# Kernel optimization log

Measured on AMD Instinct MI355X. Metric: run time of the kernel, lower is better.

Reference implementation:

```python
import jax, jax.numpy as jnp
import numpy as np

D_MODEL = 1024
N_HEADS = 16
D_HEAD = D_MODEL // N_HEADS
D_FF = 4096
BATCH = 2
SEQ = 2048
LN_EPS = 1e-5


def setup_inputs() -> dict:
    key = jax.random.key(0)
    ks = jax.random.split(key, 12)
    s = 1.0 / np.sqrt(D_MODEL)
    x = jax.random.normal(ks[0], (BATCH, SEQ, D_MODEL), dtype=jnp.float32)
    mask = jnp.broadcast_to(jnp.tril(jnp.ones((SEQ, SEQ), jnp.int32)), (BATCH, SEQ, SEQ))
    return {
        "x": x,
        "mask": mask,
        # per-head projections stacked: [H, D, Dh] (bias=False in source)
        "Wq": jax.random.normal(ks[1], (N_HEADS, D_MODEL, D_HEAD), jnp.float32) * s,
        "Wk": jax.random.normal(ks[2], (N_HEADS, D_MODEL, D_HEAD), jnp.float32) * s,
        "Wv": jax.random.normal(ks[3], (N_HEADS, D_MODEL, D_HEAD), jnp.float32) * s,
        "Wo": jax.random.normal(ks[4], (D_MODEL, D_MODEL), jnp.float32) * s,
        "ln1_w": jnp.ones((D_MODEL,), jnp.float32),
        "ln1_b": jnp.zeros((D_MODEL,), jnp.float32),
        "ln2_w": jnp.ones((D_MODEL,), jnp.float32),
        "ln2_b": jnp.zeros((D_MODEL,), jnp.float32),
        "W1": jax.random.normal(ks[5], (D_MODEL, D_FF), jnp.float32) * s,
        "b1": jnp.zeros((D_FF,), jnp.float32),
        "W2": jax.random.normal(ks[6], (D_FF, D_MODEL), jnp.float32) * (1.0 / np.sqrt(D_FF)),
        "b2": jnp.zeros((D_MODEL,), jnp.float32),
    }


def layer_norm(x, w, b):
    mu = jnp.mean(x, axis=-1, keepdims=True)
    var = jnp.var(x, axis=-1, keepdims=True)
    return (x - mu) * jax.lax.rsqrt(var + LN_EPS) * w + b


def reference(x, mask, Wq, Wk, Wv, Wo, ln1_w, ln1_b, ln2_w, ln2_b, W1, b1, W2, b2):
    # pre-LN masked self-attention
    h = layer_norm(x, ln1_w, ln1_b)
    q = jnp.einsum("bsd,hde->bhse", h, Wq)  # [B,H,S,Dh]
    k = jnp.einsum("bsd,hde->bhse", h, Wk)
    v = jnp.einsum("bsd,hde->bhse", h, Wv)
    scores = jnp.einsum("bhse,bhte->bhst", q, k) / np.sqrt(D_HEAD)
    scores = jnp.where(mask[:, None, :, :].astype(bool), scores, -jnp.inf)
    weights = jax.nn.softmax(scores, axis=-1)
    attn = jnp.einsum("bhst,bhte->bhse", weights, v)  # [B,H,S,Dh]
    # concat heads (head order = last-dim order in torch.cat)
    concat = attn.transpose(0, 2, 1, 3).reshape(x.shape[0], x.shape[1], D_MODEL)
    att_out = concat @ Wo
    att_x = x + att_out
    # FFN with exact (erf) GELU, matching nn.GELU default
    h2 = layer_norm(att_x, ln2_w, ln2_b)
    ff = jax.nn.gelu(h2 @ W1 + b1, approximate=False) @ W2 + b2
    return att_x + ff
```

## Files before the change

### kernel.cpp

```cpp
#include <hip/hip_runtime.h>
#include <hip/hip_bf16.h>
#include <math.h>

#define D_MODEL 1024
#define N_HEADS 16
#define D_HEAD  64
#define D_FF    4096
#define BATCH   2
#define SEQ     2048
#define NTOK    (BATCH*SEQ)

typedef __hip_bfloat16 bf16;
typedef __attribute__((ext_vector_type(8))) short short8;
typedef __attribute__((ext_vector_type(4))) float floatx4;

template<typename TIN>
__global__ void ln_kernel(const TIN* __restrict__ x,
                          const float* __restrict__ w,
                          const float* __restrict__ b,
                          bf16* __restrict__ out) {
    int row = blockIdx.x;
    int tid = threadIdx.x;
    const long base = (long)row * D_MODEL;
    float v[4];
    float s = 0.f, sq = 0.f;
#pragma unroll
    for (int i = 0; i < 4; ++i) {
        float xv = (float)x[base + tid + i*256];
        v[i] = xv; s += xv; sq += xv*xv;
    }
    __shared__ float r1[256], r2[256];
    r1[tid] = s; r2[tid] = sq; __syncthreads();
    for (int off = 128; off > 0; off >>= 1) {
        if (tid < off) { r1[tid] += r1[tid+off]; r2[tid] += r2[tid+off]; }
        __syncthreads();
    }
    float mean = r1[0] * (1.f/D_MODEL);
    float var  = r2[0] * (1.f/D_MODEL) - mean*mean;
    float rstd = rsqrtf(var + 1e-5f);
#pragma unroll
    for (int i = 0; i < 4; ++i) {
        int c = tid + i*256;
        out[base + c] = __float2bfloat16((v[i] - mean) * rstd * w[c] + b[c]);
    }
}

__global__ __launch_bounds__(256) void wcvt_kernel(const float* __restrict__ W,
                                                   bf16* __restrict__ Wt,
                                                   int K, int N) {
    __shared__ float t[32][33];
    int n0 = blockIdx.x * 32, k0 = blockIdx.y * 32;
    int lx = threadIdx.x & 31, ly = threadIdx.x >> 5;
#pragma unroll
    for (int i = 0; i < 4; ++i) {
        int k = ly + i * 8;
        t[k][lx] = W[(long)(k0 + k) * N + n0 + lx];
    }
    __syncthreads();
#pragma unroll
    for (int i = 0; i < 4; ++i) {
        int n = ly + i * 8;
        Wt[(long)(n0 + n) * K + k0 + lx] = __float2bfloat16(t[lx][n]);
    }
}

__global__ __launch_bounds__(256) void wcvt_wo_w1(const float* __restrict__ Wo,
                                                  const float* __restrict__ W1,
                                                  bf16* __restrict__ wo_bf,
                                                  bf16* __restrict__ w1_bf) {
    __shared__ float t[32][33];
    int gx = blockIdx.x;
    const float* W; bf16* Wt; int N, n0;
    if (gx < 32) { W = Wo; Wt = wo_bf; N = D_MODEL; n0 = gx * 32; }
    else         { W = W1; Wt = w1_bf; N = D_FF;    n0 = (gx - 32) * 32; }
    int k0 = blockIdx.y * 32;
    int lx = threadIdx.x & 31, ly = threadIdx.x >> 5;
#pragma unroll
    for (int i = 0; i < 4; ++i) {
        int k = ly + i * 8;
        t[k][lx] = W[(long)(k0 + k) * N + n0 + lx];
    }
    __syncthreads();
#pragma unroll
    for (int i = 0; i < 4; ++i) {
        int n = ly + i * 8;
        Wt[(long)(n0 + n) * D_MODEL + k0 + lx] = __float2bfloat16(t[lx][n]);
    }
}

__global__ __launch_bounds__(256) void wcvt_qkv(const float* __restrict__ Wq,
                                                const float* __restrict__ Wk,
                                                const float* __restrict__ Wv,
                                                bf16* __restrict__ outp) {
    __shared__ float t[32][33];
    int z = blockIdx.z, mat = z >> 4, head = z & 15;
    const float* W = (mat == 0 ? Wq : mat == 1 ? Wk : Wv) + (long)head * D_MODEL * D_HEAD;
    bf16* Wt = outp + (long)z * D_HEAD * D_MODEL;
    int n0 = blockIdx.x * 32, k0 = blockIdx.y * 32;
    int lx = threadIdx.x & 31, ly = threadIdx.x >> 5;
#pragma unroll
    for (int i = 0; i < 4; ++i) {
        int k = ly + i * 8;
        t[k][lx] = W[(long)(k0 + k) * D_HEAD + n0 + lx];
    }
    __syncthreads();
#pragma unroll
    for (int i = 0; i < 4; ++i) {
        int n = ly + i * 8;
        Wt[(long)(n0 + n) * D_MODEL + k0 + lx] = __float2bfloat16(t[lx][n]);
    }
}

template<int ROWS>
__device__ inline void stage_tile(const bf16* g, int gstride, short* lds) {
    int lane = threadIdx.x & 63, wave = threadIdx.x >> 6;
#pragma unroll
    for (int it = 0; it < ROWS / 64; ++it) {
        int c = wave + it * 4;
        const bf16* gp = g + (long)(c * 16 + (lane >> 2)) * gstride + (lane & 3) * 8;
        short* lp = lds + c * 512 + lane * 8;
        __builtin_amdgcn_global_load_lds(
            (const __attribute__((address_space(1))) void*)gp,
            (__attribute__((address_space(3))) void*)lp, 16, 0, 0);
    }
}

template<int BM, int BN>
__device__ inline void gemm_accum(const bf16* __restrict__ A, int lda,
                                  const bf16* __restrict__ Wt, int K,
                                  int row0, int col0, short* As, short* Bs,
                                  floatx4 (&acc)[BM/32][BN/32]) {
    constexpr int MI = BM / 32;
    constexpr int NR = BN / 32;
    int tid  = threadIdx.x;
    int wave = tid >> 6, lane = tid & 63;
    int quad = lane >> 4, l16 = lane & 15;
    int wm = (wave >> 1) * (BM / 2);
    int wn = (wave & 1) * (BN / 2);

    for (int k0 = 0; k0 < K; k0 += 64) {
        stage_tile<BM>(A  + (long)row0 * lda + k0,      lda, As);
        stage_tile<BM>(A  + (long)row0 * lda + k0 + 32, lda, As + BM * 32);
        stage_tile<BN>(Wt + (long)col0 * K   + k0,      K,   Bs);
        stage_tile<BN>(Wt + (long)col0 * K   + k0 + 32, K,   Bs + BN * 32);
        __syncthreads();

#pragma unroll
        for (int p = 0; p < 2; ++p) {
            const short* Ap = As + p * BM * 32;
            const short* Bp = Bs + p * BN * 32;
            short8 af[MI], bfr[NR];
#pragma unroll
            for (int mi = 0; mi < MI; ++mi)
                af[mi] = *(const short8*)&Ap[(wm + mi * 16 + l16) * 32 + quad * 8];
#pragma unroll
            for (int ni = 0; ni < NR; ++ni)
                bfr[ni] = *(const short8*)&Bp[(wn + ni * 16 + l16) * 32 + quad * 8];
#pragma unroll
            for (int mi = 0; mi < MI; ++mi)
#pragma unroll
                for (int ni = 0; ni < NR; ++ni)
                    acc[mi][ni] = __builtin_amdgcn_mfma_f32_16x16x32_bf16(
                        af[mi], bfr[ni], acc[mi][ni], 0, 0, 0);
        }
        __syncthreads();
    }
}

template<int BM, int BN, int BIAS, int ACT, int RES, int OUTBF16>
__global__ __launch_bounds__(256) void mfma_gemm_bf(
    const bf16* __restrict__ A, int lda,
    const bf16* __restrict__ Wt, int K,
    const float* __restrict__ bias, const float* __restrict__ resid,
    void* __restrict__ Cout, int ldc)
{
    constexpr int MI = BM / 32;
    constexpr int NR = BN / 32;
    __shared__ short As[BM * 64];
    __shared__ short Bs[BN * 64];
    int row0 = blockIdx.y * BM, col0 = blockIdx.x * BN;
    int tid = threadIdx.x, wave = tid >> 6, lane = tid & 63;
    int quad = lane >> 4, l16 = lane & 15;
    int wm = (wave >> 1) * (BM / 2);
    int wn = (wave & 1) * (BN / 2);

    floatx4 acc[MI][NR];
#pragma unroll
    for (int mi = 0; mi < MI; ++mi)
#pragma unroll
        for (int ni = 0; ni < NR; ++ni)
            acc[mi][ni] = (floatx4){0.f, 0.f, 0.f, 0.f};

    gemm_accum<BM, BN>(A, lda, Wt, K, row0, col0, As, Bs, acc);

#pragma unroll
    for (int mi = 0; mi < MI; ++mi) {
#pragma unroll
        for (int ni = 0; ni < NR; ++ni) {
#pragma unroll
            for (int r = 0; r < 4; ++r) {
                int row = row0 + wm + mi * 16 + quad * 4 + r;
                int col = col0 + wn + ni * 16 + l16;
                float v = acc[mi][ni][r];
                if (BIAS) v += bias[col];
                if (ACT == 1) {
                    float x2 = v * v;
                    float arg = fminf(v * fmaf(0.1029392f, x2, 2.3021182f), 20.f);
                    float t = exp2f(arg);
                    v = v * t * __builtin_amdgcn_rcpf(t + 1.f);
                }
                long idx = (long)row * ldc + col;
                if (RES == 1) v += resid[idx];
                if (OUTBF16) ((bf16*)Cout)[idx] = __float2bfloat16(v);
                else         ((float*)Cout)[idx] = v;
            }
        }
    }
}

struct QkvOut { bf16* o[3]; };
__global__ __launch_bounds__(256) void qkv_kernel(const bf16* __restrict__ h1,
                                                  const bf16* __restrict__ wqkv,
                                                  QkvOut a) {
    __shared__ short As[128 * 64];
    __shared__ short Bs[128 * 64];
    int row0 = blockIdx.y * 128, col0 = blockIdx.x * 128;
    int tid = threadIdx.x, wave = tid >> 6, lane = tid & 63;
    int quad = lane >> 4, l16 = lane & 15;
    int wm = (wave >> 1) * 64, wn = (wave & 1) * 64;

    floatx4 acc[4][4];
#pragma unroll
    for (int mi = 0; mi < 4; ++mi)
#pragma unroll
        for (int ni = 0; ni < 4; ++ni)
            acc[mi][ni] = (floatx4){0.f, 0.f, 0.f, 0.f};

    gemm_accum<128, 128>(h1, D_MODEL, wqkv, D_MODEL, row0, col0, As, Bs, acc);

#pragma unroll
    for (int mi = 0; mi < 4; ++mi) {
#pragma unroll
        for (int ni = 0; ni < 4; ++ni) {
#pragma unroll
            for (int r = 0; r < 4; ++r) {
                int row = row0 + wm + mi * 16 + quad * 4 + r;
                int c   = col0 + wn + ni * 16 + l16;
                int mat = c >> 10, hd = (c >> 6) & 15, d = c & 63;
                int b = row >> 11, s = row & 2047;
                a.o[mat][(((long)(b * 16 + hd) * SEQ + s) << 6) + d] =
                    __float2bfloat16(acc[mi][ni][r]);
            }
        }
    }
}

__global__ __launch_bounds__(256) void fattn_mfma(const bf16* __restrict__ q,
                                                  const bf16* __restrict__ k,
                                                  const bf16* __restrict__ v,
                                                  bf16* __restrict__ po,
                                                  float* __restrict__ lz) {
    int byr = blockIdx.y;
    int tile = (byr < 8) ? byr : 23 - byr;
    int chunk = blockIdx.z;
    int bh = blockIdx.x;
    int tid = threadIdx.x;
    int wave = tid >> 6, lane = tid & 63;
    int quad = lane >> 4, l16 = lane & 15;
    const long base = (long)bh * SEQ * D_HEAD;
    const int r0g = tile * 128;

    bf16*  pob = po + (long)chunk * 32 * SEQ * 64;
    float* lzb = lz + (long)chunk * 32 * SEQ;

    __shared__ short Ks[64 * 72];
    __shared__ short Vt[64 * 72];
    __shared__ short Ps[4][32 * 72];

    short8 qf[2][2];
#pragma unroll
    for (int rb = 0; rb < 2; ++rb) {
        const short* qrow = (const short*)(q + base +
            (long)(r0g + wave * 32 + rb * 16 + l16) * D_HEAD);
        qf[rb][0] = *(const short8*)(qrow + quad * 8);
        qf[rb][1] = *(const short8*)(qrow + 32 + quad * 8);
#pragma unroll
        for (int c = 0; c < 2; ++c)
#pragma unroll
            for (int j = 0; j < 8; ++j) {
                float f = __uint_as_float(((unsigned)(unsigned short)qf[rb][c][j]) << 16)
                          * 0.18033688f;
                qf[rb][c][j] = __builtin_bit_cast(short, __float2bfloat16(f));
            }
    }

    short8 onesf;
    {
        short o1 = (l16 == 0) ? (short)0x3F80 : (short)0;
#pragma unroll
        for (int j = 0; j < 8; ++j) onesf[j] = o1;
    }

    floatx4 o[2][4];
#pragma unroll
    for (int rb = 0; rb < 2; ++rb)
#pragma unroll
        for (int nb = 0; nb < 4; ++nb) o[rb][nb] = (floatx4){0.f, 0.f, 0.f, 0.f};
    floatx4 l4[2] = {(floatx4){0.f,0.f,0.f,0.f}, (floatx4){0.f,0.f,0.f,0.f}};

    const int kt0 = chunk ? tile + 1 : 0;
    const int kt1 = chunk ? 2 * tile + 1 : tile;
    for (int kt = kt0; kt <= kt1; ++kt) {
        __syncthreads();
        {
            int t = tid >> 2, c = tid & 3;
            const short* krow = (const short*)(k + base + (long)(kt * 64 + t) * D_HEAD);
            *(uint4*)&Ks[t * 72 + c * 16]     = *(const uint4*)(krow + c * 16);
            *(uint4*)&Ks[t * 72 + c * 16 + 8] = *(const uint4*)(krow + c * 16 + 8);
        }
        {
            int tp = (tid & 31) * 2;
            int d0 = ((tid >> 5) & 7) * 8;
            const short* v0 = (const short*)(v + base + (long)(kt * 64 + tp) * D_HEAD + d0);
            short va[8], vb[8];
            *(uint4*)va = *(const uint4*)v0;
            *(uint4*)vb = *(const uint4*)(v0 + D_HEAD);
#pragma unroll
            for (int j = 0; j < 8; ++j) {
                unsigned pk = (unsigned)(unsigned short)va[j] |
                              ((unsigned)(unsigned short)vb[j] << 16);
                *(unsigned*)&Vt[(d0 + j) * 72 + tp] = pk;
            }
        }
        __syncthreads();

        if (kt * 64 > r0g + wave * 32 + 31) continue;

        floatx4 s[2][4];
#pragma unroll
        for (int nb = 0; nb < 4; ++nb) {
            short8 kf0 = *(const short8*)&Ks[(nb * 16 + l16) * 72 + quad * 8];
            short8 kf1 = *(const short8*)&Ks[(nb * 16 + l16) * 72 + 32 + quad * 8];
#pragma unroll
            for (int rb = 0; rb < 2; ++rb) {
                floatx4 z4 = (floatx4){0.f, 0.f, 0.f, 0.f};
                z4 = __builtin_amdgcn_mfma_f32_16x16x32_bf16(qf[rb][0], kf0, z4, 0, 0, 0);
                z4 = __builtin_amdgcn_mfma_f32_16x16x32_bf16(qf[rb][1], kf1, z4, 0, 0, 0);
                s[rb][nb] = z4;
            }
        }

        if (kt >= 2 * tile) {
#pragma unroll
            for (int rb = 0; rb < 2; ++rb) {
                int qg = r0g + wave * 32 + rb * 16 + quad * 4;
#pragma unroll
                for (int nb = 0; nb < 4; ++nb) {
                    int kg = kt * 64 + nb * 16 + l16;
#pragma unroll
                    for (int r = 0; r < 4; ++r)
                        if (kg > qg + r) s[rb][nb][r] = -1e30f;
                }
            }
        }

        short* Pw = &Ps[wave][0];
#pragma unroll
        for (int rb = 0; rb < 2; ++rb)
#pragma unroll
            for (int nb = 0; nb < 4; ++nb)
#pragma unroll
                for (int r = 0; r < 4; ++r) {
                    float p = exp2f(s[rb][nb][r]);
                    Pw[(rb * 16 + quad * 4 + r) * 72 + nb * 16 + l16] =
                        __builtin_bit_cast(short, __float2bfloat16(p));
                }

        short8 pf[2][2];
#pragma unroll
        for (int rb = 0; rb < 2; ++rb) {
            pf[rb][0] = *(const short8*)&Pw[(rb * 16 + l16) * 72 + quad * 8];
            pf[rb][1] = *(const short8*)&Pw[(rb * 16 + l16) * 72 + 32 + quad * 8];
        }
#pragma unroll
        for (int nb = 0; nb < 4; ++nb) {
            short8 vf0 = *(const short8*)&Vt[(nb * 16 + l16) * 72 + quad * 8];
            short8 vf1 = *(const short8*)&Vt[(nb * 16 + l16) * 72 + 32 + quad * 8];
#pragma unroll
            for (int rb = 0; rb < 2; ++rb) {
                o[rb][nb] = __builtin_amdgcn_mfma_f32_16x16x32_bf16(pf[rb][0], vf0, o[rb][nb], 0, 0, 0);
                o[rb][nb] = __builtin_amdgcn_mfma_f32_16x16x32_bf16(pf[rb][1], vf1, o[rb][nb], 0, 0, 0);
            }
        }
#pragma unroll
        for (int rb = 0; rb < 2; ++rb) {
            l4[rb] = __builtin_amdgcn_mfma_f32_16x16x32_bf16(pf[rb][0], onesf, l4[rb], 0, 0, 0);
            l4[rb] = __builtin_amdgcn_mfma_f32_16x16x32_bf16(pf[rb][1], onesf, l4[rb], 0, 0, 0);
        }
    }

#pragma unroll
    for (int rb = 0; rb < 2; ++rb) {
#pragma unroll
        for (int nb = 0; nb < 4; ++nb)
#pragma unroll
            for (int r = 0; r < 4; ++r) {
                int row = r0g + wave * 32 + rb * 16 + quad * 4 + r;
                pob[((long)bh * SEQ + row) * 64 + nb * 16 + l16] =
                    __float2bfloat16(o[rb][nb][r]);
            }
        if (l16 == 0) {
#pragma unroll
            for (int r = 0; r < 4; ++r) {
                int row = r0g + wave * 32 + rb * 16 + quad * 4 + r;
                lzb[(long)bh * SEQ + row] = l4[rb][r];
            }
        }
    }
}

__global__ __launch_bounds__(256) void attn_combine(const bf16* __restrict__ po,
                                                    const float* __restrict__ lz,
                                                    bf16* __restrict__ cc) {
    const long CH = 32L * SEQ * 64;
    int row = blockIdx.x;
    int b = row >> 11, s = row & 2047;
    int tid = threadIdx.x;
    int col = tid * 4;
    int h = col >> 6, d = col & 63;
    long pidx = ((long)(b * 16 + h) * SEQ + s) * 64 + d;
    uint2 u0 = *(const uint2*)((const unsigned short*)po + pidx);
    uint2 u1 = *(const uint2*)((const unsigned short*)po + CH + pidx);
    long li = (long)(b * 16 + h) * SEQ + s;
    float linv = 1.f / (lz[li] + lz[32L * SEQ + li]);
    unsigned ua[4] = {u0.x & 0xFFFFu, u0.x >> 16, u0.y & 0xFFFFu, u0.y >> 16};
    unsigned ub[4] = {u1.x & 0xFFFFu, u1.x >> 16, u1.y & 0xFFFFu, u1.y >> 16};
    unsigned short rr[4];
#pragma unroll
    for (int i = 0; i < 4; ++i) {
        float ov = __uint_as_float(ua[i] << 16) + __uint_as_float(ub[i] << 16);
        rr[i] = __builtin_bit_cast(unsigned short, __float2bfloat16(ov * linv));
    }
    uint2 w;
    w.x = (unsigned)rr[0] | ((unsigned)rr[1] << 16);
    w.y = (unsigned)rr[2] | ((unsigned)rr[3] << 16);
    *(uint2*)((unsigned short*)cc + (long)row * D_MODEL + col) = w;
}

extern "C" void kernel_launch(void* const* d_in, const int* in_sizes, int n_in,
                              void* d_out, int out_size, void* d_ws, size_t ws_size,
                              hipStream_t stream) {
    const float* x    = (const float*)d_in[0];
    const float* Wq   = (const float*)d_in[2];
    const float* Wk   = (const float*)d_in[3];
    const float* Wv   = (const float*)d_in[4];
    const float* Wo   = (const float*)d_in[5];
    const float* ln1w = (const float*)d_in[6];
    const float* ln1b = (const float*)d_in[7];
    const float* ln2w = (const float*)d_in[8];
    const float* ln2b = (const float*)d_in[9];
    const float* W1   = (const float*)d_in[10];
    const float* b1   = (const float*)d_in[11];
    const float* W2   = (const float*)d_in[12];
    const float* b2   = (const float*)d_in[13];
    float* out = (float*)d_out;

    char* wsb = (char*)d_ws;
    const size_t MB = 1024*1024;
    bf16*  h1      = (bf16*)(wsb + 0*MB);
    bf16*  qb      = (bf16*)(wsb + 8*MB);
    bf16*  kb      = (bf16*)(wsb + 16*MB);
    bf16*  vb      = (bf16*)(wsb + 24*MB);
    bf16*  wqkv_bf = (bf16*)(wsb + 32*MB);
    bf16*  po      = (bf16*)(wsb + 32*MB);
    float* lz      = (float*)(wsb + 48*MB);
    bf16*  cc      = (bf16*)(wsb + 0*MB);
    bf16*  wo_bf   = (bf16*)(wsb + 8*MB);
    bf16*  w1_bf   = (bf16*)(wsb + 10*MB);
    bf16*  h2      = (bf16*)(wsb + 0*MB);
    bf16*  ff      = (bf16*)(wsb + 24*MB);
    bf16*  w2_bf   = (bf16*)(wsb + 8*MB);

    ln_kernel<float><<<NTOK, 256, 0, stream>>>(x, ln1w, ln1b, h1);

    wcvt_qkv<<<dim3(2, 32, 48), 256, 0, stream>>>(Wq, Wk, Wv, wqkv_bf);

    QkvOut qa; qa.o[0] = qb; qa.o[1] = kb; qa.o[2] = vb;
    qkv_kernel<<<dim3(24, 32), 256, 0, stream>>>(h1, wqkv_bf, qa);

    fattn_mfma<<<dim3(BATCH*N_HEADS, SEQ/128, 2), 256, 0, stream>>>(qb, kb, vb, po, lz);

    attn_combine<<<NTOK, 256, 0, stream>>>(po, lz, cc);

    wcvt_wo_w1<<<dim3(160, 32), 256, 0, stream>>>(Wo, W1, wo_bf, w1_bf);

    mfma_gemm_bf<64,128,0,0,1,0><<<dim3(8,64), 256, 0, stream>>>(
        cc, D_MODEL, wo_bf, D_MODEL, nullptr, x, out, D_MODEL);

    ln_kernel<float><<<NTOK, 256, 0, stream>>>(out, ln2w, ln2b, h2);

    mfma_gemm_bf<128,128,1,1,0,1><<<dim3(32,32), 256, 0, stream>>>(
        h2, D_MODEL, w1_bf, D_MODEL, b1, nullptr, ff, D_FF);

    wcvt_kernel<<<dim3(D_MODEL/32, D_FF/32), 256, 0, stream>>>(W2, w2_bf, D_FF, D_MODEL);

    mfma_gemm_bf<64,128,1,0,1,0><<<dim3(8,64), 256, 0, stream>>>(
        ff, D_FF, w2_bf, D_FF, b2, out, out, D_MODEL);
}
```

Measured before the change: 381.7 us.

## Double-buffer GEMM LDS tiles and remap workgroups for XCD locality

The shared GEMM main loop now double-buffers its LDS tiles. The next K-slice is issued with global_load_lds while MFMAs run on the current buffer, so there is one barrier per iteration instead of two. To keep LDS use in check, K-depth is a template parameter: 32 for the 128x128 tiles (QKV and W1) and 64 for the 64x128 tiles. All GEMM kernels also remap block IDs so consecutive tiles land on the same XCD, improving L2 reuse. The smaller K-step on the large tiles means more loop iterations and barriers, and prefetch overlap depends on the barrier's vmcnt wait.

```diff
diff --git a/kernel.cpp b/kernel.cpp
--- a/kernel.cpp
+++ b/kernel.cpp
@@ -111,6 +111,15 @@
     }
 }
 
+__device__ inline void swz2d(int& bx, int& by) {
+    int gx = gridDim.x;
+    int nwg = gx * gridDim.y;
+    int bid = blockIdx.y * gx + blockIdx.x;
+    int swz = (bid & 7) * (nwg >> 3) + (bid >> 3);
+    bx = swz % gx;
+    by = swz / gx;
+}
+
 template<int ROWS>
 __device__ inline void stage_tile(const bf16* g, int gstride, short* lds) {
     int lane = threadIdx.x & 63, wave = threadIdx.x >> 6;
@@ -125,30 +134,42 @@
     }
 }
 
-template<int BM, int BN>
+template<int BM, int BN, int BK>
 __device__ inline void gemm_accum(const bf16* __restrict__ A, int lda,
                                   const bf16* __restrict__ Wt, int K,
                                   int row0, int col0, short* As, short* Bs,
                                   floatx4 (&acc)[BM/32][BN/32]) {
-    constexpr int MI = BM / 32;
-    constexpr int NR = BN / 32;
+    constexpr int MI  = BM / 32;
+    constexpr int NR  = BN / 32;
+    constexpr int ASZ = BM * BK;
+    constexpr int BSZ = BN * BK;
     int tid  = threadIdx.x;
     int wave = tid >> 6, lane = tid & 63;
     int quad = lane >> 4, l16 = lane & 15;
     int wm = (wave >> 1) * (BM / 2);
     int wn = (wave & 1) * (BN / 2);
 
-    for (int k0 = 0; k0 < K; k0 += 64) {
-        stage_tile<BM>(A  + (long)row0 * lda + k0,      lda, As);
-        stage_tile<BM>(A  + (long)row0 * lda + k0 + 32, lda, As + BM * 32);
-        stage_tile<BN>(Wt + (long)col0 * K   + k0,      K,   Bs);
-        stage_tile<BN>(Wt + (long)col0 * K   + k0 + 32, K,   Bs + BN * 32);
-        __syncthreads();
-
-#pragma unroll
-        for (int p = 0; p < 2; ++p) {
-            const short* Ap = As + p * BM * 32;
-            const short* Bp = Bs + p * BN * 32;
+    auto stage = [&](int k0, int buf) {
+#pragma unroll
+        for (int kk = 0; kk < BK; kk += 32) {
+            stage_tile<BM>(A  + (long)row0 * lda + k0 + kk, lda,
+                           As + buf * ASZ + (kk / 32) * BM * 32);
+            stage_tile<BN>(Wt + (long)col0 * K   + k0 + kk, K,
+                           Bs + buf * BSZ + (kk / 32) * BN * 32);
+        }
+    };
+
+    stage(0, 0);
+    __syncthreads();
+
+    int cur = 0;
+    for (int k0 = 0; k0 < K; k0 += BK) {
+        if (k0 + BK < K) stage(k0 + BK, cur ^ 1);
+
+#pragma unroll
+        for (int p = 0; p < BK / 32; ++p) {
+            const short* Ap = As + cur * ASZ + p * BM * 32;
+            const short* Bp = Bs + cur * BSZ + p * BN * 32;
             short8 af[MI], bfr[NR];
 #pragma unroll
             for (int mi = 0; mi < MI; ++mi)
@@ -164,10 +185,11 @@
                         af[mi], bfr[ni], acc[mi][ni], 0, 0, 0);
         }
         __syncthreads();
-    }
-}
-
-template<int BM, int BN, int BIAS, int ACT, int RES, int OUTBF16>
+        cur ^= 1;
+    }
+}
+
+template<int BM, int BN, int BK, int BIAS, int ACT, int RES, int OUTBF16>
 __global__ __launch_bounds__(256) void mfma_gemm_bf(
     const bf16* __restrict__ A, int lda,
     const bf16* __restrict__ Wt, int K,
@@ -176,9 +198,10 @@
 {
     constexpr int MI = BM / 32;
     constexpr int NR = BN / 32;
-    __shared__ short As[BM * 64];
-    __shared__ short Bs[BN * 64];
-    int row0 = blockIdx.y * BM, col0 = blockIdx.x * BN;
+    __shared__ short As[2 * BM * BK];
+    __shared__ short Bs[2 * BN * BK];
+    int bx, by; swz2d(bx, by);
+    int row0 = by * BM, col0 = bx * BN;
     int tid = threadIdx.x, wave = tid >> 6, lane = tid & 63;
     int quad = lane >> 4, l16 = lane & 15;
     int wm = (wave >> 1) * (BM / 2);
@@ -191,7 +214,7 @@
         for (int ni = 0; ni < NR; ++ni)
             acc[mi][ni] = (floatx4){0.f, 0.f, 0.f, 0.f};
 
-    gemm_accum<BM, BN>(A, lda, Wt, K, row0, col0, As, Bs, acc);
+    gemm_accum<BM, BN, BK>(A, lda, Wt, K, row0, col0, As, Bs, acc);
 
 #pragma unroll
     for (int mi = 0; mi < MI; ++mi) {
@@ -222,9 +245,10 @@
 __global__ __launch_bounds__(256) void qkv_kernel(const bf16* __restrict__ h1,
                                                   const bf16* __restrict__ wqkv,
                                                   QkvOut a) {
-    __shared__ short As[128 * 64];
-    __shared__ short Bs[128 * 64];
-    int row0 = blockIdx.y * 128, col0 = blockIdx.x * 128;
+    __shared__ short As[2 * 128 * 32];
+    __shared__ short Bs[2 * 128 * 32];
+    int bx, by; swz2d(bx, by);
+    int row0 = by * 128, col0 = bx * 128;
     int tid = threadIdx.x, wave = tid >> 6, lane = tid & 63;
     int quad = lane >> 4, l16 = lane & 15;
     int wm = (wave >> 1) * 64, wn = (wave & 1) * 64;
@@ -236,7 +260,7 @@
         for (int ni = 0; ni < 4; ++ni)
             acc[mi][ni] = (floatx4){0.f, 0.f, 0.f, 0.f};
 
-    gemm_accum<128, 128>(h1, D_MODEL, wqkv, D_MODEL, row0, col0, As, Bs, acc);
+    gemm_accum<128, 128, 32>(h1, D_MODEL, wqkv, D_MODEL, row0, col0, As, Bs, acc);
 
 #pragma unroll
     for (int mi = 0; mi < 4; ++mi) {
@@ -494,16 +518,16 @@
 
     wcvt_wo_w1<<<dim3(160, 32), 256, 0, stream>>>(Wo, W1, wo_bf, w1_bf);
 
-    mfma_gemm_bf<64,128,0,0,1,0><<<dim3(8,64), 256, 0, stream>>>(
+    mfma_gemm_bf<64,128,64,0,0,1,0><<<dim3(8,64), 256, 0, stream>>>(
         cc, D_MODEL, wo_bf, D_MODEL, nullptr, x, out, D_MODEL);
 
     ln_kernel<float><<<NTOK, 256, 0, stream>>>(out, ln2w, ln2b, h2);
 
-    mfma_gemm_bf<128,128,1,1,0,1><<<dim3(32,32), 256, 0, stream>>>(
+    mfma_gemm_bf<128,128,32,1,1,0,1><<<dim3(32,32), 256, 0, stream>>>(
         h2, D_MODEL, w1_bf, D_MODEL, b1, nullptr, ff, D_FF);
 
     wcvt_kernel<<<dim3(D_MODEL/32, D_FF/32), 256, 0, stream>>>(W2, w2_bf, D_FF, D_MODEL);
 
-    mfma_gemm_bf<64,128,1,0,1,0><<<dim3(8,64), 256, 0, stream>>>(
+    mfma_gemm_bf<64,128,64,1,0,1,0><<<dim3(8,64), 256, 0, stream>>>(
         ff, D_FF, w2_bf, D_FF, b2, out, out, D_MODEL);
 }
```

After: 381.9 us. No clear change (+0.1%).
